# Kernel tuning notes

Hardware: AMD Instinct MI355X
Metric: run time of the kernel (lower is better)

## Reference

```python
import jax, jax.numpy as jnp
import numpy as np

INPUT_SIZE = 784
HIDDEN_SIZE = 256
NUM_CLASSES = 10
BATCH = 32768


def setup_inputs() -> dict:
    key = jax.random.key(0)
    k_x, k_w1, k_b1, k_w2, k_b2 = jax.random.split(key, 5)
    return {
        "x": jax.random.normal(k_x, (BATCH, INPUT_SIZE), dtype=jnp.float32),
        "fc1_weight": jax.random.normal(k_w1, (HIDDEN_SIZE, INPUT_SIZE), dtype=jnp.float32),
        "fc1_bias": jax.random.normal(k_b1, (HIDDEN_SIZE,), dtype=jnp.float32),
        "fc2_weight": jax.random.normal(k_w2, (NUM_CLASSES, HIDDEN_SIZE), dtype=jnp.float32),
        "fc2_bias": jax.random.normal(k_b2, (NUM_CLASSES,), dtype=jnp.float32),
    }


def reference(x, fc1_weight, fc1_bias, fc2_weight, fc2_bias):
    # hidden = x @ W1^T + b1, ReLU
    hidden = jnp.einsum("bi,hi->bh", x, fc1_weight) + fc1_bias
    activated = jnp.maximum(hidden, 0.0)
    # output = activated @ W2^T + b2
    logits = jnp.einsum("bh,ch->bc", activated, fc2_weight) + fc2_bias
    return jax.nn.softmax(logits, axis=-1)
```

## Files before the change

### kernel.cpp

```cpp
#include <hip/hip_runtime.h>
#include <math.h>

#define BATCH_N   32768
#define IN_F      784
#define HID_F     256
#define NCLS      10
#define BM        64
#define BK        32
#define NKT       25
#define NTHREADS  256

typedef __attribute__((ext_vector_type(8))) short short8;
typedef __attribute__((ext_vector_type(4))) float f32x4;

#define WS_W1H 0
#define WS_W1L 409600

union S8U { short8 s; uint4 u; };

__device__ __forceinline__ void cvt8(float4 a, float4 b, short8* hi, short8* lo) {
    const unsigned M = 0xFFFF0000u;
    const unsigned ux = __float_as_uint(a.x), uy = __float_as_uint(a.y),
                   uz = __float_as_uint(a.z), uw = __float_as_uint(a.w),
                   vx = __float_as_uint(b.x), vy = __float_as_uint(b.y),
                   vz = __float_as_uint(b.z), vw = __float_as_uint(b.w);
    S8U h, l;
    h.u.x = (ux >> 16) | (uy & M);
    h.u.y = (uz >> 16) | (uw & M);
    h.u.z = (vx >> 16) | (vy & M);
    h.u.w = (vz >> 16) | (vw & M);
    const float rx = a.x - __uint_as_float(ux & M);
    const float ry = a.y - __uint_as_float(uy & M);
    const float rz = a.z - __uint_as_float(uz & M);
    const float rw = a.w - __uint_as_float(uw & M);
    const float sx = b.x - __uint_as_float(vx & M);
    const float sy = b.y - __uint_as_float(vy & M);
    const float sz = b.z - __uint_as_float(vz & M);
    const float sw_ = b.w - __uint_as_float(vw & M);
    l.u.x = (__float_as_uint(rx) >> 16) | (__float_as_uint(ry) & M);
    l.u.y = (__float_as_uint(rz) >> 16) | (__float_as_uint(rw) & M);
    l.u.z = (__float_as_uint(sx) >> 16) | (__float_as_uint(sy) & M);
    l.u.w = (__float_as_uint(sz) >> 16) | (__float_as_uint(sw_) & M);
    *hi = h.s; *lo = l.s;
}

__global__ __launch_bounds__(256)
void prep_w1_kernel(const float* __restrict__ w1, char* __restrict__ ws) {
    const int s    = blockIdx.x * 256 + threadIdx.x;
    const int lane = s & 63, ct = (s >> 6) & 15, kt = s >> 10;
    const int n    = ct * 16 + (lane & 15);
    const int k0   = kt * 32 + (lane >> 4) * 8;
    float4 a = make_float4(0.f, 0.f, 0.f, 0.f), b = a;
    if (k0 + 7 < IN_F) {
        const float* p = w1 + (size_t)n * IN_F + k0;
        a = *(const float4*)p;
        b = *(const float4*)(p + 4);
    }
    short8 hi, lo;
    cvt8(a, b, &hi, &lo);
    *(short8*)(ws + WS_W1H + (size_t)s * 16) = hi;
    *(short8*)(ws + WS_W1L + (size_t)s * 16) = lo;
}

__global__ __launch_bounds__(NTHREADS, 2)
void mlp_mfma_kernel(const float* __restrict__ x,
                     const char*  __restrict__ wsb,
                     const float* __restrict__ b1,
                     const float* __restrict__ w2,
                     const float* __restrict__ b2,
                     float* __restrict__ out)
{
    __shared__ float hid[BM * HID_F];

    const int tid  = threadIdx.x;
    const int wv   = tid >> 6;
    const int lane = tid & 63;
    const int m    = lane & 15;
    const int quad = lane >> 4;
    const int row0 = blockIdx.x * BM;
    const int kq   = quad * 8;

    f32x4 acc[4][4];
    #pragma unroll
    for (int a = 0; a < 4; ++a)
        #pragma unroll
        for (int b = 0; b < 4; ++b)
            acc[a][b] = (f32x4){0.f, 0.f, 0.f, 0.f};

    const float* xb[4];
    #pragma unroll
    for (int rt = 0; rt < 4; ++rt)
        xb[rt] = x + (size_t)(row0 + rt * 16 + m) * IN_F;

    const char* bhp = wsb + WS_W1H + ((size_t)(wv * 4) * 64 + lane) * 16;
    const char* blp = wsb + WS_W1L + ((size_t)(wv * 4) * 64 + lane) * 16;

    float4 xc[4][2];
    #pragma unroll
    for (int rt = 0; rt < 4; ++rt) {
        xc[rt][0] = *(const float4*)(xb[rt] + kq);
        xc[rt][1] = *(const float4*)(xb[rt] + kq + 4);
    }

    #pragma unroll 4
    for (int kt = 0; kt < NKT - 1; ++kt) {
        short8 bh[4], bl[4];
        #pragma unroll
        for (int c = 0; c < 4; ++c) {
            bh[c] = *(const short8*)(bhp + (size_t)kt * 16384 + c * 1024);
            bl[c] = *(const short8*)(blp + (size_t)kt * 16384 + c * 1024);
        }
        int kon = (kt + 1) * BK + kq;
        kon = kon > (IN_F - 8) ? (IN_F - 8) : kon;
        float4 xn[4][2];
        #pragma unroll
        for (int rt = 0; rt < 4; ++rt) {
            xn[rt][0] = *(const float4*)(xb[rt] + kon);
            xn[rt][1] = *(const float4*)(xb[rt] + kon + 4);
        }
        short8 ah[4], al[4];
        #pragma unroll
        for (int rt = 0; rt < 4; ++rt)
            cvt8(xc[rt][0], xc[rt][1], &ah[rt], &al[rt]);
        #pragma unroll
        for (int rt = 0; rt < 4; ++rt)
            #pragma unroll
            for (int c = 0; c < 4; ++c) {
                acc[rt][c] = __builtin_amdgcn_mfma_f32_16x16x32_bf16(ah[rt], bh[c], acc[rt][c], 0, 0, 0);
                acc[rt][c] = __builtin_amdgcn_mfma_f32_16x16x32_bf16(al[rt], bh[c], acc[rt][c], 0, 0, 0);
                acc[rt][c] = __builtin_amdgcn_mfma_f32_16x16x32_bf16(ah[rt], bl[c], acc[rt][c], 0, 0, 0);
            }
        #pragma unroll
        for (int rt = 0; rt < 4; ++rt) {
            xc[rt][0] = xn[rt][0];
            xc[rt][1] = xn[rt][1];
        }
    }

    {
        const int kt = NKT - 1;
        short8 bh[4], bl[4];
        #pragma unroll
        for (int c = 0; c < 4; ++c) {
            bh[c] = *(const short8*)(bhp + (size_t)kt * 16384 + c * 1024);
            bl[c] = *(const short8*)(blp + (size_t)kt * 16384 + c * 1024);
        }
        short8 ah[4], al[4];
        #pragma unroll
        for (int rt = 0; rt < 4; ++rt)
            cvt8(xc[rt][0], xc[rt][1], &ah[rt], &al[rt]);
        if (quad >= 2) {
            const short8 zz = {0, 0, 0, 0, 0, 0, 0, 0};
            #pragma unroll
            for (int rt = 0; rt < 4; ++rt) { ah[rt] = zz; al[rt] = zz; }
        }
        #pragma unroll
        for (int rt = 0; rt < 4; ++rt)
            #pragma unroll
            for (int c = 0; c < 4; ++c) {
                acc[rt][c] = __builtin_amdgcn_mfma_f32_16x16x32_bf16(ah[rt], bh[c], acc[rt][c], 0, 0, 0);
                acc[rt][c] = __builtin_amdgcn_mfma_f32_16x16x32_bf16(al[rt], bh[c], acc[rt][c], 0, 0, 0);
                acc[rt][c] = __builtin_amdgcn_mfma_f32_16x16x32_bf16(ah[rt], bl[c], acc[rt][c], 0, 0, 0);
            }
    }

    #pragma unroll
    for (int c = 0; c < 4; ++c) {
        const int col = (wv * 4 + c) * 16 + m;
        const float bv = b1[col];
        #pragma unroll
        for (int rt = 0; rt < 4; ++rt)
            #pragma unroll
            for (int reg = 0; reg < 4; ++reg) {
                const int row = rt * 16 + quad * 4 + reg;
                hid[row * 256 + (col ^ ((row & 7) << 2))] = fmaxf(acc[rt][c][reg] + bv, 0.f);
            }
    }
    __syncthreads();

    const int rl = wv * 16 + m;
    const int sw = (rl & 7) << 2;
    const float* hrow = hid + rl * 256;
    float lg[NCLS];
    #pragma unroll
    for (int c = 0; c < NCLS; ++c) lg[c] = 0.f;
    #pragma unroll
    for (int i = 0; i < 8; ++i) {
        const int h0 = i * 32 + quad * 8;
        const float4 h1 = *(const float4*)(hrow + (h0 ^ sw));
        const float4 h2 = *(const float4*)(hrow + ((h0 + 4) ^ sw));
        #pragma unroll
        for (int c = 0; c < NCLS; ++c) {
            const float4 wa = *(const float4*)(w2 + c * HID_F + h0);
            const float4 wb = *(const float4*)(w2 + c * HID_F + h0 + 4);
            lg[c] += h1.x * wa.x + h1.y * wa.y + h1.z * wa.z + h1.w * wa.w
                   + h2.x * wb.x + h2.y * wb.y + h2.z * wb.z + h2.w * wb.w;
        }
    }
    #pragma unroll
    for (int c = 0; c < NCLS; ++c) {
        float v = lg[c];
        v += __shfl_xor(v, 16);
        v += __shfl_xor(v, 32);
        lg[c] = v;
    }
    if (quad == 0) {
        float mx = -1e30f;
        #pragma unroll
        for (int c = 0; c < NCLS; ++c) { lg[c] += b2[c]; mx = fmaxf(mx, lg[c]); }
        float s = 0.f;
        #pragma unroll
        for (int c = 0; c < NCLS; ++c) { lg[c] = __expf(lg[c] - mx); s += lg[c]; }
        const float inv = 1.f / s;
        float* o = out + (size_t)(row0 + rl) * NCLS;
        #pragma unroll
        for (int c = 0; c < NCLS; ++c) o[c] = lg[c] * inv;
    }
}

extern "C" void kernel_launch(void* const* d_in, const int* in_sizes, int n_in,
                              void* d_out, int out_size, void* d_ws, size_t ws_size,
                              hipStream_t stream)
{
    const float* x  = (const float*)d_in[0];
    const float* w1 = (const float*)d_in[1];
    const float* b1 = (const float*)d_in[2];
    const float* w2 = (const float*)d_in[3];
    const float* b2 = (const float*)d_in[4];
    float* out = (float*)d_out;

    hipLaunchKernelGGL(prep_w1_kernel, dim3(100), dim3(256), 0, stream,
                       w1, (char*)d_ws);
    hipLaunchKernelGGL(mlp_mfma_kernel, dim3(BATCH_N / BM), dim3(NTHREADS), 0, stream,
                       x, (const char*)d_ws, b1, w2, b2, out);
}
```

Baseline: 201.0 us.

## Fuse fc2 into MFMA epilogue and split block into 8 waves

Each block now uses 8 waves arranged as 2 row groups by 4 column groups, so each wave holds half as many accumulators, and occupancy is raised to 4 blocks per SM. The second layer is computed directly from the MFMA accumulators in registers: each lane multiplies its ReLU'd hidden values by W2, reduces across lanes with shuffles, and writes only small per-column-group partial logits to shared memory. This replaces the 64 KB hidden-activation LDS buffer and its reload. The x register double-buffering prefetch is dropped, which risks exposing more global-load latency and adds many shuffles in the epilogue.

New measurement: 232.5 us. +15.7%, slower.

```diff
diff --git a/kernel.cpp b/kernel.cpp
--- a/kernel.cpp
+++ b/kernel.cpp
@@ -8,7 +8,7 @@
 #define BM        64
 #define BK        32
 #define NKT       25
-#define NTHREADS  256
+#define NTHREADS  512
 
 typedef __attribute__((ext_vector_type(8))) short short8;
 typedef __attribute__((ext_vector_type(4))) float f32x4;
@@ -62,7 +62,7 @@
     *(short8*)(ws + WS_W1L + (size_t)s * 16) = lo;
 }
 
-__global__ __launch_bounds__(NTHREADS, 2)
+__global__ __launch_bounds__(NTHREADS, 4)
 void mlp_mfma_kernel(const float* __restrict__ x,
                      const char*  __restrict__ wsb,
                      const float* __restrict__ b1,
@@ -70,71 +70,57 @@
                      const float* __restrict__ b2,
                      float* __restrict__ out)
 {
-    __shared__ float hid[BM * HID_F];
+    __shared__ float part[4][BM][NCLS + 2];
 
     const int tid  = threadIdx.x;
-    const int wv   = tid >> 6;
+    const int w    = tid >> 6;
+    const int rg   = w >> 2;
+    const int cg   = w & 3;
     const int lane = tid & 63;
     const int m    = lane & 15;
     const int quad = lane >> 4;
+    const int kq   = quad * 8;
     const int row0 = blockIdx.x * BM;
-    const int kq   = quad * 8;
-
-    f32x4 acc[4][4];
-    #pragma unroll
-    for (int a = 0; a < 4; ++a)
+
+    f32x4 acc[2][4];
+    #pragma unroll
+    for (int a = 0; a < 2; ++a)
         #pragma unroll
         for (int b = 0; b < 4; ++b)
             acc[a][b] = (f32x4){0.f, 0.f, 0.f, 0.f};
 
-    const float* xb[4];
-    #pragma unroll
-    for (int rt = 0; rt < 4; ++rt)
-        xb[rt] = x + (size_t)(row0 + rt * 16 + m) * IN_F;
-
-    const char* bhp = wsb + WS_W1H + ((size_t)(wv * 4) * 64 + lane) * 16;
-    const char* blp = wsb + WS_W1L + ((size_t)(wv * 4) * 64 + lane) * 16;
-
-    float4 xc[4][2];
-    #pragma unroll
-    for (int rt = 0; rt < 4; ++rt) {
-        xc[rt][0] = *(const float4*)(xb[rt] + kq);
-        xc[rt][1] = *(const float4*)(xb[rt] + kq + 4);
-    }
+    const float* xb[2];
+    #pragma unroll
+    for (int rt = 0; rt < 2; ++rt)
+        xb[rt] = x + (size_t)(row0 + rg * 32 + rt * 16 + m) * IN_F;
+
+    const char* bhp = wsb + WS_W1H + ((size_t)(cg * 4) * 64 + lane) * 16;
+    const char* blp = wsb + WS_W1L + ((size_t)(cg * 4) * 64 + lane) * 16;
 
     #pragma unroll 4
     for (int kt = 0; kt < NKT - 1; ++kt) {
+        const int kb = kt * BK;
         short8 bh[4], bl[4];
         #pragma unroll
         for (int c = 0; c < 4; ++c) {
             bh[c] = *(const short8*)(bhp + (size_t)kt * 16384 + c * 1024);
             bl[c] = *(const short8*)(blp + (size_t)kt * 16384 + c * 1024);
         }
-        int kon = (kt + 1) * BK + kq;
-        kon = kon > (IN_F - 8) ? (IN_F - 8) : kon;
-        float4 xn[4][2];
-        #pragma unroll
-        for (int rt = 0; rt < 4; ++rt) {
-            xn[rt][0] = *(const float4*)(xb[rt] + kon);
-            xn[rt][1] = *(const float4*)(xb[rt] + kon + 4);
-        }
-        short8 ah[4], al[4];
-        #pragma unroll
-        for (int rt = 0; rt < 4; ++rt)
-            cvt8(xc[rt][0], xc[rt][1], &ah[rt], &al[rt]);
-        #pragma unroll
-        for (int rt = 0; rt < 4; ++rt)
+        short8 ah[2], al[2];
+        #pragma unroll
+        for (int rt = 0; rt < 2; ++rt) {
+            const float4 a0 = *(const float4*)(xb[rt] + kb + kq);
+            const float4 a1 = *(const float4*)(xb[rt] + kb + kq + 4);
+            cvt8(a0, a1, &ah[rt], &al[rt]);
+        }
+        #pragma unroll
+        for (int rt = 0; rt < 2; ++rt)
             #pragma unroll
             for (int c = 0; c < 4; ++c) {
                 acc[rt][c] = __builtin_amdgcn_mfma_f32_16x16x32_bf16(ah[rt], bh[c], acc[rt][c], 0, 0, 0);
                 acc[rt][c] = __builtin_amdgcn_mfma_f32_16x16x32_bf16(al[rt], bh[c], acc[rt][c], 0, 0, 0);
                 acc[rt][c] = __builtin_amdgcn_mfma_f32_16x16x32_bf16(ah[rt], bl[c], acc[rt][c], 0, 0, 0);
             }
-        #pragma unroll
-        for (int rt = 0; rt < 4; ++rt) {
-            xc[rt][0] = xn[rt][0];
-            xc[rt][1] = xn[rt][1];
-        }
     }
 
     {
@@ -145,17 +131,21 @@
             bh[c] = *(const short8*)(bhp + (size_t)kt * 16384 + c * 1024);
             bl[c] = *(const short8*)(blp + (size_t)kt * 16384 + c * 1024);
         }
-        short8 ah[4], al[4];
-        #pragma unroll
-        for (int rt = 0; rt < 4; ++rt)
-            cvt8(xc[rt][0], xc[rt][1], &ah[rt], &al[rt]);
+        const int kon = (768 + kq) > (IN_F - 8) ? (IN_F - 8) : (768 + kq);
+        short8 ah[2], al[2];
+        #pragma unroll
+        for (int rt = 0; rt < 2; ++rt) {
+            const float4 a0 = *(const float4*)(xb[rt] + kon);
+            const float4 a1 = *(const float4*)(xb[rt] + kon + 4);
+            cvt8(a0, a1, &ah[rt], &al[rt]);
+        }
         if (quad >= 2) {
             const short8 zz = {0, 0, 0, 0, 0, 0, 0, 0};
             #pragma unroll
-            for (int rt = 0; rt < 4; ++rt) { ah[rt] = zz; al[rt] = zz; }
-        }
-        #pragma unroll
-        for (int rt = 0; rt < 4; ++rt)
+            for (int rt = 0; rt < 2; ++rt) { ah[rt] = zz; al[rt] = zz; }
+        }
+        #pragma unroll
+        for (int rt = 0; rt < 2; ++rt)
             #pragma unroll
             for (int c = 0; c < 4; ++c) {
                 acc[rt][c] = __builtin_amdgcn_mfma_f32_16x16x32_bf16(ah[rt], bh[c], acc[rt][c], 0, 0, 0);
@@ -164,57 +154,78 @@
             }
     }
 
-    #pragma unroll
-    for (int c = 0; c < 4; ++c) {
-        const int col = (wv * 4 + c) * 16 + m;
-        const float bv = b1[col];
-        #pragma unroll
-        for (int rt = 0; rt < 4; ++rt)
+    float w2v[4][NCLS], b1v[4];
+    #pragma unroll
+    for (int ct = 0; ct < 4; ++ct) {
+        const int col = (cg * 4 + ct) * 16 + m;
+        b1v[ct] = b1[col];
+        #pragma unroll
+        for (int c = 0; c < NCLS; ++c)
+            w2v[ct][c] = w2[c * HID_F + col];
+    }
+    #pragma unroll
+    for (int rt = 0; rt < 2; ++rt) {
+        float p[4][NCLS];
+        #pragma unroll
+        for (int reg = 0; reg < 4; ++reg)
+            #pragma unroll
+            for (int c = 0; c < NCLS; ++c) p[reg][c] = 0.f;
+        #pragma unroll
+        for (int ct = 0; ct < 4; ++ct)
             #pragma unroll
             for (int reg = 0; reg < 4; ++reg) {
-                const int row = rt * 16 + quad * 4 + reg;
-                hid[row * 256 + (col ^ ((row & 7) << 2))] = fmaxf(acc[rt][c][reg] + bv, 0.f);
-            }
+                const float h = fmaxf(acc[rt][ct][reg] + b1v[ct], 0.f);
+                #pragma unroll
+                for (int c = 0; c < NCLS; ++c) p[reg][c] += h * w2v[ct][c];
+            }
+        #pragma unroll
+        for (int reg = 0; reg < 4; ++reg)
+            #pragma unroll
+            for (int c = 0; c < NCLS; ++c) {
+                float v = p[reg][c];
+                v += __shfl_xor(v, 1);
+                v += __shfl_xor(v, 2);
+                v += __shfl_xor(v, 4);
+                v += __shfl_xor(v, 8);
+                p[reg][c] = v;
+            }
+        if (m == 0) {
+            #pragma unroll
+            for (int reg = 0; reg < 4; ++reg) {
+                const int row = rg * 32 + rt * 16 + quad * 4 + reg;
+                #pragma unroll
+                for (int c = 0; c < NCLS; ++c)
+                    part[cg][row][c] = p[reg][c];
+            }
+        }
     }
     __syncthreads();
 
-    const int rl = wv * 16 + m;
-    const int sw = (rl & 7) << 2;
-    const float* hrow = hid + rl * 256;
-    float lg[NCLS];
-    #pragma unroll
-    for (int c = 0; c < NCLS; ++c) lg[c] = 0.f;
-    #pragma unroll
-    for (int i = 0; i < 8; ++i) {
-        const int h0 = i * 32 + quad * 8;
-        const float4 h1 = *(const float4*)(hrow + (h0 ^ sw));
-        const float4 h2 = *(const float4*)(hrow + ((h0 + 4) ^ sw));
+    if (tid < 4 * BM) {
+        const int row = tid >> 2;
+        const int cgi = tid & 3;
+        float lg[NCLS];
+        #pragma unroll
+        for (int c = 0; c < NCLS; ++c) lg[c] = part[cgi][row][c];
         #pragma unroll
         for (int c = 0; c < NCLS; ++c) {
-            const float4 wa = *(const float4*)(w2 + c * HID_F + h0);
-            const float4 wb = *(const float4*)(w2 + c * HID_F + h0 + 4);
-            lg[c] += h1.x * wa.x + h1.y * wa.y + h1.z * wa.z + h1.w * wa.w
-                   + h2.x * wb.x + h2.y * wb.y + h2.z * wb.z + h2.w * wb.w;
-        }
-    }
-    #pragma unroll
-    for (int c = 0; c < NCLS; ++c) {
-        float v = lg[c];
-        v += __shfl_xor(v, 16);
-        v += __shfl_xor(v, 32);
-        lg[c] = v;
-    }
-    if (quad == 0) {
-        float mx = -1e30f;
-        #pragma unroll
-        for (int c = 0; c < NCLS; ++c) { lg[c] += b2[c]; mx = fmaxf(mx, lg[c]); }
-        float s = 0.f;
-        #pragma unroll
-        for (int c = 0; c < NCLS; ++c) { lg[c] = __expf(lg[c] - mx); s += lg[c]; }
-        const float inv = 1.f / s;
-        float* o = out + (size_t)(row0 + rl) * NCLS;
-        #pragma unroll
-        for (int c = 0; c < NCLS; ++c) o[c] = lg[c] * inv;
+            float v = lg[c];
+            v += __shfl_xor(v, 1);
+            v += __shfl_xor(v, 2);
+            lg[c] = v;
+        }
+        if (cgi == 0) {
+            float mx = -1e30f;
+            #pragma unroll
+            for (int c = 0; c < NCLS; ++c) { lg[c] += b2[c]; mx = fmaxf(mx, lg[c]); }
+            float s = 0.f;
+            #pragma unroll
+            for (int c = 0; c < NCLS; ++c) { lg[c] = __expf(lg[c] - mx); s += lg[c]; }
+            const float inv = 1.f / s;
+            float* o = out + (size_t)(row0 + row) * NCLS;
+            #pragma unroll
+            for (int c = 0; c < NCLS; ++c) o[c] = lg[c] * inv;
+        }
     }
 }
 
```
